# Performance work log

Measured on AMD Instinct MI355X. Metric: run time of the kernel, lower is better.

The kernel has to match this reference:

```python
import jax, jax.numpy as jnp
import numpy as np

N = 50000
E = 1600000
D_IN = 128
HID = 128
EPS = 1e-5
NEG_SLOPE = 0.2


def setup_inputs() -> dict:
    key = jax.random.key(0)
    ks = jax.random.split(key, 16)
    s = 1.0 / np.sqrt(D_IN)
    inp = {
        'x': jax.random.normal(ks[0], (N, D_IN), dtype=jnp.float32),
        'edge_index': jax.random.randint(ks[1], (2, E), 0, N, dtype=jnp.int64),
        # layer 0 params
        'W0': jax.random.normal(ks[2], (D_IN, HID), dtype=jnp.float32) * s,
        'att_src0': jax.random.normal(ks[3], (HID,), dtype=jnp.float32) * s,
        'att_dst0': jax.random.normal(ks[4], (HID,), dtype=jnp.float32) * s,
        'bias0': jnp.zeros((HID,), dtype=jnp.float32),
        'gamma0': jnp.ones((HID,), dtype=jnp.float32),
        'beta0': jnp.zeros((HID,), dtype=jnp.float32),
        # layer 1 params
        'W1': jax.random.normal(ks[5], (HID, HID), dtype=jnp.float32) * s,
        'att_src1': jax.random.normal(ks[6], (HID,), dtype=jnp.float32) * s,
        'att_dst1': jax.random.normal(ks[7], (HID,), dtype=jnp.float32) * s,
        'bias1': jnp.zeros((HID,), dtype=jnp.float32),
        'gamma1': jnp.ones((HID,), dtype=jnp.float32),
        'beta1': jnp.zeros((HID,), dtype=jnp.float32),
    }
    return inp


def _gat_conv(x, W, a_src, a_dst, bias, src, dst, n_nodes):
    h = x @ W                                   # [N, HID]
    alpha_src = h @ a_src                       # [N]
    alpha_dst = h @ a_dst                       # [N]
    e = jax.nn.leaky_relu(alpha_src[src] + alpha_dst[dst], NEG_SLOPE)  # [E']
    # numerically stable softmax over edges grouped by destination node
    m = jax.ops.segment_max(e, dst, num_segments=n_nodes)
    ex = jnp.exp(e - m[dst])
    denom = jax.ops.segment_sum(ex, dst, num_segments=n_nodes)
    alpha = ex / denom[dst]                     # [E']
    out = jax.ops.segment_sum(h[src] * alpha[:, None], dst, num_segments=n_nodes)
    return out + bias


def _batch_norm(x, gamma, beta):
    mean = jnp.mean(x, axis=0)
    var = jnp.mean(jnp.square(x - mean), axis=0)  # biased variance (torch BN normalization)
    return gamma * (x - mean) * jax.lax.rsqrt(var + EPS) + beta


def reference(x, edge_index, W0, att_src0, att_dst0, bias0, gamma0, beta0,
              W1, att_src1, att_dst1, bias1, gamma1, beta1):
    n = x.shape[0]
    loops = jnp.arange(n, dtype=edge_index.dtype)
    src = jnp.concatenate([edge_index[0], loops])
    dst = jnp.concatenate([edge_index[1], loops])

    h = _gat_conv(x, W0, att_src0, att_dst0, bias0, src, dst, n)
    h = _batch_norm(h, gamma0, beta0)
    h = jax.nn.relu(h)
    # dropout: identity in eval mode

    h = _gat_conv(h, W1, att_src1, att_dst1, bias1, src, dst, n)
    h = _batch_norm(h, gamma1, beta1)
    h = jax.nn.relu(h)  # last_activation=True
    return h
```

## Files before the change

kernel.cpp:

```cpp
#include <hip/hip_runtime.h>
#include <math.h>

#define HID 128
#define PAD 96
#define NB 196
#define CAP 10240
#define CHUNK 4096
#define AGG_BLOCKS 2048
#define NEG_SLOPE 0.2f
#define EPS 1e-5f

typedef __attribute__((ext_vector_type(8))) short short8;
typedef __attribute__((ext_vector_type(4))) float floatx4;

static __device__ __forceinline__ unsigned bf16_rne(float x) {
    unsigned u = __float_as_uint(x);
    return (u + 0x7fffu + ((u >> 16) & 1u)) >> 16;
}
static __device__ __forceinline__ float bf16lo_f(unsigned u) { return __uint_as_float(u << 16); }
static __device__ __forceinline__ float bf16hi_f(unsigned u) { return __uint_as_float(u & 0xffff0000u); }

__global__ void wt_build(const float* __restrict__ W, unsigned short* __restrict__ Wt,
                         unsigned short* __restrict__ Hb, int N) {
    int t = threadIdx.x;
    if (t < 64) ((unsigned*)(Hb + (size_t)N * HID))[t] = 0u;
    for (int task = t; task < 2048; task += 256) {
        int c = task & 127, k0 = (task >> 7) * 8;
        unsigned v[8];
#pragma unroll
        for (int j = 0; j < 8; ++j) v[j] = bf16_rne(W[(k0 + j) * HID + c]);
        uint4 st;
        st.x = v[0] | (v[1] << 16);
        st.y = v[2] | (v[3] << 16);
        st.z = v[4] | (v[5] << 16);
        st.w = v[6] | (v[7] << 16);
        *(uint4*)&Wt[c * HID + k0] = st;
    }
}

template <bool BN>
__global__ __launch_bounds__(256) void gemm_mfma(
    const float* __restrict__ X, const unsigned short* __restrict__ Wt,
    const float* __restrict__ a_src, const float* __restrict__ a_dst,
    const float* __restrict__ coef,
    unsigned short* __restrict__ Hb, float* __restrict__ asrc, float* __restrict__ adst,
    int N)
{
    int tid = threadIdx.x;
    int wv = tid >> 6, lane = tid & 63;
    int g = lane >> 4, c = lane & 15;
    int r0w = blockIdx.x * 64 + wv * 16;
    int arow = r0w + c;
    bool avalid = arow < N;
    const float* xr = X + (size_t)(avalid ? arow : 0) * HID;

    floatx4 acc[8];
#pragma unroll
    for (int i = 0; i < 8; ++i) acc[i] = (floatx4)0.f;

#pragma unroll
    for (int kc = 0; kc < 4; ++kc) {
        int k0 = kc * 32 + g * 8;
        float xv[8];
        float4 x0 = *(const float4*)&xr[k0];
        float4 x1 = *(const float4*)&xr[k0 + 4];
        xv[0] = x0.x; xv[1] = x0.y; xv[2] = x0.z; xv[3] = x0.w;
        xv[4] = x1.x; xv[5] = x1.y; xv[6] = x1.z; xv[7] = x1.w;
        if (BN) {
            float4 s0 = *(const float4*)&coef[k0];
            float4 s1 = *(const float4*)&coef[k0 + 4];
            float4 h0 = *(const float4*)&coef[HID + k0];
            float4 h1 = *(const float4*)&coef[HID + k0 + 4];
            xv[0] = fmaxf(fmaf(xv[0], s0.x, h0.x), 0.f);
            xv[1] = fmaxf(fmaf(xv[1], s0.y, h0.y), 0.f);
            xv[2] = fmaxf(fmaf(xv[2], s0.z, h0.z), 0.f);
            xv[3] = fmaxf(fmaf(xv[3], s0.w, h0.w), 0.f);
            xv[4] = fmaxf(fmaf(xv[4], s1.x, h1.x), 0.f);
            xv[5] = fmaxf(fmaf(xv[5], s1.y, h1.y), 0.f);
            xv[6] = fmaxf(fmaf(xv[6], s1.z, h1.z), 0.f);
            xv[7] = fmaxf(fmaf(xv[7], s1.w, h1.w), 0.f);
        }
        short8 af;
#pragma unroll
        for (int j = 0; j < 8; ++j) af[j] = avalid ? (short)bf16_rne(xv[j]) : (short)0;

#pragma unroll
        for (int nt = 0; nt < 8; ++nt) {
            short8 bf = *(const short8*)&Wt[(nt * 16 + c) * HID + k0];
            acc[nt] = __builtin_amdgcn_mfma_f32_16x16x32_bf16(af, bf, acc[nt], 0, 0, 0);
        }
    }

    float as_c[8], ad_c[8];
#pragma unroll
    for (int nt = 0; nt < 8; ++nt) {
        as_c[nt] = a_src[nt * 16 + c];
        ad_c[nt] = a_dst[nt * 16 + c];
    }
#pragma unroll
    for (int reg = 0; reg < 4; ++reg) {
        float s = 0.f, d = 0.f;
#pragma unroll
        for (int nt = 0; nt < 8; ++nt) {
            s = fmaf(acc[nt][reg], as_c[nt], s);
            d = fmaf(acc[nt][reg], ad_c[nt], d);
        }
#pragma unroll
        for (int o = 1; o < 16; o <<= 1) {
            s += __shfl_xor(s, o);
            d += __shfl_xor(d, o);
        }
        int crow = r0w + g * 4 + reg;
        if (c == 0 && crow < N) { asrc[crow] = s; adst[crow] = d; }
    }
#pragma unroll
    for (int reg = 0; reg < 4; ++reg) {
        int crow = r0w + g * 4 + reg;
        if (crow < N) {
#pragma unroll
            for (int nt = 0; nt < 8; ++nt)
                Hb[(size_t)crow * HID + nt * 16 + c] = (unsigned short)bf16_rne(acc[nt][reg]);
        }
    }
}

__global__ __launch_bounds__(256) void scatter_part(
    const int* __restrict__ ei, int* __restrict__ bcur,
    unsigned int* __restrict__ bbuf, int E)
{
    __shared__ int lcnt[NB], gbase[NB];
    int tid = threadIdx.x;
    int i0 = blockIdx.x * CHUNK;
    int i1 = i0 + CHUNK; if (i1 > E) i1 = E;
    if (tid < NB) lcnt[tid] = 0;
    __syncthreads();
    for (int i = i0 + tid; i < i1; i += 256)
        atomicAdd(&lcnt[ei[E + i] >> 8], 1);
    __syncthreads();
    if (tid < NB) {
        gbase[tid] = atomicAdd(&bcur[tid], lcnt[tid]);
        lcnt[tid] = 0;
    }
    __syncthreads();
    for (int i = i0 + tid; i < i1; i += 256) {
        int s = ei[i], d = ei[E + i];
        int b = d >> 8;
        int off = atomicAdd(&lcnt[b], 1);
        int pos = gbase[b] + off;
        if (pos < CAP)
            bbuf[(size_t)b * CAP + pos] = ((unsigned)s << 8) | (unsigned)(d & 255);
    }
}

__global__ __launch_bounds__(256) void ell_build(
    const unsigned int* __restrict__ bbuf, const int* __restrict__ bcur,
    int* __restrict__ cnt, int* __restrict__ ell, float* __restrict__ asrc, int N)
{
    __shared__ int stage[256 * PAD];
    __shared__ int scnt[256];
    int tid = threadIdx.x;
    int b = blockIdx.x;
    int base = b << 8;
    int nodes = N - base; if (nodes > 256) nodes = 256;

    if (b == 0 && tid == 0) asrc[N] = -1e30f;

    int4 s4; s4.x = s4.y = s4.z = s4.w = N;
    for (int idx = tid * 4; idx < 256 * PAD; idx += 1024)
        *(int4*)&stage[idx] = s4;
    __syncthreads();
    for (int i = tid; i < nodes; i += 256) {
        stage[i * PAD] = base + i;
        scnt[i] = 1;
    }
    __syncthreads();

    int nb = bcur[b]; if (nb > CAP) nb = CAP;
    const unsigned int* buf = bbuf + (size_t)b * CAP;
    for (int j = tid; j < nb; j += 256) {
        unsigned int v = buf[j];
        int dl = (int)(v & 255u);
        int s = (int)(v >> 8);
        int p = atomicAdd(&scnt[dl], 1);
        if (p < PAD) stage[dl * PAD + p] = s;
    }
    __syncthreads();

    int total = nodes * PAD;
    int* dst = ell + (size_t)base * PAD;
    for (int idx = tid * 4; idx < total; idx += 1024)
        *(int4*)&dst[idx] = *(const int4*)&stage[idx];
    for (int i = tid; i < nodes; i += 256)
        cnt[base + i] = scnt[i];
}

__global__ __launch_bounds__(256) void gat_aggregate(
    const unsigned short* __restrict__ Hb, const float* __restrict__ asrc,
    const float* __restrict__ adst, const int* __restrict__ cnt,
    const int* __restrict__ ell, const float* __restrict__ bias,
    float* __restrict__ OUT, float* __restrict__ stat, int N)
{
    __shared__ float sbuf[4][HID], qbuf[4][HID];
    int tid = threadIdx.x, wv = tid >> 6, lane = tid & 63;
    int h = lane >> 5, li = lane & 31;
    int c0 = 4 * li;
    float4 b4 = *(const float4*)&bias[c0];
    float ss0 = 0.f, ss1 = 0.f, ss2 = 0.f, ss3 = 0.f;
    float qq0 = 0.f, qq1 = 0.f, qq2 = 0.f, qq3 = 0.f;

    for (int n = blockIdx.x * 4 + wv; n < N; n += AGG_BLOCKS * 4) {
        int nn = __builtin_amdgcn_readfirstlane(n);
        int deg = cnt[nn]; if (deg > PAD) deg = PAD;
        const int* row = ell + (size_t)nn * PAD;
        float adn = adst[nn];
        float a0 = 0.f, a1 = 0.f, a2 = 0.f, a3 = 0.f, den = 0.f;

        for (int j = 0; j < deg; j += 16) {
            int4 s0 = *(const int4*)&row[j];
            int4 s1 = *(const int4*)&row[j + 4];
            int4 s2 = *(const int4*)&row[j + 8];
            int4 s3 = *(const int4*)&row[j + 12];
            int e0 = h ? s0.y : s0.x;
            int e1 = h ? s0.w : s0.z;
            int e2 = h ? s1.y : s1.x;
            int e3 = h ? s1.w : s1.z;
            int e4 = h ? s2.y : s2.x;
            int e5 = h ? s2.w : s2.z;
            int e6 = h ? s3.y : s3.x;
            int e7 = h ? s3.w : s3.z;
#define PAIR(SI) { int si = (SI);                                     \
            float v = asrc[si] + adn;                                 \
            v = fmaxf(v, v * NEG_SLOPE);                              \
            float w = __expf(v);                                      \
            den += w;                                                 \
            uint2 hv = *(const uint2*)(Hb + (size_t)si * HID + c0);   \
            a0 = fmaf(w, bf16lo_f(hv.x), a0);                         \
            a1 = fmaf(w, bf16hi_f(hv.x), a1);                         \
            a2 = fmaf(w, bf16lo_f(hv.y), a2);                         \
            a3 = fmaf(w, bf16hi_f(hv.y), a3); }
            PAIR(e0) PAIR(e1) PAIR(e2) PAIR(e3)
            PAIR(e4) PAIR(e5) PAIR(e6) PAIR(e7)
#undef PAIR
        }

        den += __shfl_xor(den, 32);
        a0 += __shfl_xor(a0, 32);
        a1 += __shfl_xor(a1, 32);
        a2 += __shfl_xor(a2, 32);
        a3 += __shfl_xor(a3, 32);

        float inv = 1.f / den;
        float o0 = fmaf(a0, inv, b4.x);
        float o1 = fmaf(a1, inv, b4.y);
        float o2 = fmaf(a2, inv, b4.z);
        float o3 = fmaf(a3, inv, b4.w);
        ss0 += o0; ss1 += o1; ss2 += o2; ss3 += o3;
        qq0 = fmaf(o0, o0, qq0); qq1 = fmaf(o1, o1, qq1);
        qq2 = fmaf(o2, o2, qq2); qq3 = fmaf(o3, o3, qq3);
        if (h == 0) {
            float4 st;
            st.x = o0; st.y = o1; st.z = o2; st.w = o3;
            *(float4*)&OUT[(size_t)nn * HID + c0] = st;
        }
    }

    if (h == 0) {
        sbuf[wv][c0] = ss0; sbuf[wv][c0 + 1] = ss1;
        sbuf[wv][c0 + 2] = ss2; sbuf[wv][c0 + 3] = ss3;
        qbuf[wv][c0] = qq0; qbuf[wv][c0 + 1] = qq1;
        qbuf[wv][c0 + 2] = qq2; qbuf[wv][c0 + 3] = qq3;
    }
    __syncthreads();
    if (tid < HID) {
        float t = sbuf[0][tid] + sbuf[1][tid] + sbuf[2][tid] + sbuf[3][tid];
        atomicAdd(&stat[tid], t);
    } else {
        int cc = tid - HID;
        float t = qbuf[0][cc] + qbuf[1][cc] + qbuf[2][cc] + qbuf[3][cc];
        atomicAdd(&stat[HID + cc], t);
    }
}

__global__ void bn_coef(const float* __restrict__ stat, const float* __restrict__ gamma,
                        const float* __restrict__ beta, float* __restrict__ coef,
                        float invN)
{
    int c = threadIdx.x;
    float mean = stat[c] * invN;
    float var = stat[HID + c] * invN - mean * mean;
    float s = gamma[c] * rsqrtf(var + EPS);
    coef[c] = s;
    coef[HID + c] = beta[c] - mean * s;
}

__global__ __launch_bounds__(256) void bn_apply(
    float* __restrict__ X, const float* __restrict__ coef, int N)
{
    int tid = threadIdx.x, lane = tid & 63, wv = tid >> 6;
    int c0 = 2 * lane;
    float s0 = coef[c0], s1 = coef[c0 + 1];
    float h0 = coef[HID + c0], h1 = coef[HID + c0 + 1];
    for (int r = blockIdx.x * 4 + wv; r < N; r += gridDim.x * 4) {
        float2 v = *(float2*)&X[(size_t)r * HID + c0];
        float y0 = fmaxf(fmaf(v.x, s0, h0), 0.f);
        float y1 = fmaxf(fmaf(v.y, s1, h1), 0.f);
        *(float2*)&X[(size_t)r * HID + c0] = make_float2(y0, y1);
    }
}

extern "C" void kernel_launch(void* const* d_in, const int* in_sizes, int n_in,
                              void* d_out, int out_size, void* d_ws, size_t ws_size,
                              hipStream_t stream)
{
    const float* x        = (const float*)d_in[0];
    const int*   ei       = (const int*)d_in[1];
    const float* W0       = (const float*)d_in[2];
    const float* att_src0 = (const float*)d_in[3];
    const float* att_dst0 = (const float*)d_in[4];
    const float* bias0    = (const float*)d_in[5];
    const float* gamma0   = (const float*)d_in[6];
    const float* beta0    = (const float*)d_in[7];
    const float* W1       = (const float*)d_in[8];
    const float* att_src1 = (const float*)d_in[9];
    const float* att_dst1 = (const float*)d_in[10];
    const float* bias1    = (const float*)d_in[11];
    const float* gamma1   = (const float*)d_in[12];
    const float* beta1    = (const float*)d_in[13];

    const int N = in_sizes[0] / HID;
    const int E = in_sizes[1] / 2;
    float* out = (float*)d_out;

    char* wsbase = (char*)d_ws;
    size_t off = 0;
    auto alloc = [&](size_t bytes) -> void* {
        void* p = wsbase + off;
        off += (bytes + 255) & ~(size_t)255;
        return p;
    };
    unsigned short* Hb   = (unsigned short*)alloc((size_t)(N + 1) * HID * 2);
    float*          asrc = (float*)alloc((size_t)(N + 1) * 4);
    float*          adst = (float*)alloc((size_t)N * 4);
    int*            cnt  = (int*)  alloc((size_t)N * 4);
    int*            ell  = (int*)  alloc((size_t)N * PAD * 4);
    unsigned int*   bbuf = (unsigned int*)alloc((size_t)NB * CAP * 4);
    int*            bcur = (int*)  alloc(NB * 4);
    float*          stats = (float*)alloc(4 * HID * 4);
    float*          coef0 = (float*)alloc(2 * HID * 4);
    float*          coef1 = (float*)alloc(2 * HID * 4);
    unsigned short* Wt0  = (unsigned short*)alloc(HID * HID * 2);
    unsigned short* Wt1  = (unsigned short*)alloc(HID * HID * 2);
    float* stat0 = stats;
    float* stat1 = stats + 2 * HID;

    const int gemm_blocks  = (N + 63) / 64;
    const int part_blocks  = (E + CHUNK - 1) / CHUNK;
    const int build_blocks = (N + 255) / 256;
    const float invN = 1.0f / (float)N;

    (void)hipMemsetAsync(bcur, 0, NB * 4, stream);
    (void)hipMemsetAsync(stats, 0, 4 * HID * 4, stream);

    wt_build<<<1, 256, 0, stream>>>(W0, Wt0, Hb, N);
    wt_build<<<1, 256, 0, stream>>>(W1, Wt1, Hb, N);
    scatter_part<<<part_blocks, 256, 0, stream>>>(ei, bcur, bbuf, E);
    ell_build<<<build_blocks, 256, 0, stream>>>(bbuf, bcur, cnt, ell, asrc, N);

    gemm_mfma<false><<<gemm_blocks, 256, 0, stream>>>(
        x, Wt0, att_src0, att_dst0, nullptr, Hb, asrc, adst, N);
    gat_aggregate<<<AGG_BLOCKS, 256, 0, stream>>>(
        Hb, asrc, adst, cnt, ell, bias0, out, stat0, N);
    bn_coef<<<1, HID, 0, stream>>>(stat0, gamma0, beta0, coef0, invN);

    gemm_mfma<true><<<gemm_blocks, 256, 0, stream>>>(
        out, Wt1, att_src1, att_dst1, coef0, Hb, asrc, adst, N);
    gat_aggregate<<<AGG_BLOCKS, 256, 0, stream>>>(
        Hb, asrc, adst, cnt, ell, bias1, out, stat1, N);
    bn_coef<<<1, HID, 0, stream>>>(stat1, gamma1, beta1, coef1, invN);
    bn_apply<<<2048, 256, 0, stream>>>(out, coef1, N);
}
```

Before: 289.9 us.

## Precompute packed per-edge attention weights before GAT aggregation

Adds an edge_w kernel that computes the leaky-ReLU exp attention weight for every padded ELL slot. It packs each weight as bf16 together with the 16-bit source index into one word. The aggregation kernel then reads these packed words, dropping its per-edge asrc gather and exp, and the aggregation grid size is doubled. In exchange the new kernel touches every padded slot, which is about three times the real edge count, and adds a full read and write of the ELL array per layer. It also narrows the weights to bf16 and relies on node indices fitting in 16 bits.

New measurement: 382.8 us. 32.1% more time.

```diff
diff --git a/kernel.cpp b/kernel.cpp
--- a/kernel.cpp
+++ b/kernel.cpp
@@ -6,7 +6,7 @@
 #define NB 196
 #define CAP 10240
 #define CHUNK 4096
-#define AGG_BLOCKS 2048
+#define AGG_BLOCKS 4096
 #define NEG_SLOPE 0.2f
 #define EPS 1e-5f
 
@@ -194,10 +194,23 @@
         cnt[base + i] = scnt[i];
 }
 
+__global__ __launch_bounds__(256) void edge_w(
+    const int* __restrict__ ell, const float* __restrict__ asrc,
+    const float* __restrict__ adst, unsigned* __restrict__ ellw, int total)
+{
+    int i = blockIdx.x * 256 + threadIdx.x;
+    if (i >= total) return;
+    int si = ell[i];
+    int node = i / PAD;
+    float v = asrc[si] + adst[node];
+    v = fmaxf(v, v * NEG_SLOPE);
+    float w = __expf(v);
+    ellw[i] = ((unsigned)si << 16) | bf16_rne(w);
+}
+
 __global__ __launch_bounds__(256) void gat_aggregate(
-    const unsigned short* __restrict__ Hb, const float* __restrict__ asrc,
-    const float* __restrict__ adst, const int* __restrict__ cnt,
-    const int* __restrict__ ell, const float* __restrict__ bias,
+    const unsigned short* __restrict__ Hb, const unsigned* __restrict__ ellw,
+    const int* __restrict__ cnt, const float* __restrict__ bias,
     float* __restrict__ OUT, float* __restrict__ stat, int N)
 {
     __shared__ float sbuf[4][HID], qbuf[4][HID];
@@ -211,27 +224,25 @@
     for (int n = blockIdx.x * 4 + wv; n < N; n += AGG_BLOCKS * 4) {
         int nn = __builtin_amdgcn_readfirstlane(n);
         int deg = cnt[nn]; if (deg > PAD) deg = PAD;
-        const int* row = ell + (size_t)nn * PAD;
-        float adn = adst[nn];
+        const unsigned* row = ellw + (size_t)nn * PAD;
         float a0 = 0.f, a1 = 0.f, a2 = 0.f, a3 = 0.f, den = 0.f;
 
         for (int j = 0; j < deg; j += 16) {
-            int4 s0 = *(const int4*)&row[j];
-            int4 s1 = *(const int4*)&row[j + 4];
-            int4 s2 = *(const int4*)&row[j + 8];
-            int4 s3 = *(const int4*)&row[j + 12];
-            int e0 = h ? s0.y : s0.x;
-            int e1 = h ? s0.w : s0.z;
-            int e2 = h ? s1.y : s1.x;
-            int e3 = h ? s1.w : s1.z;
-            int e4 = h ? s2.y : s2.x;
-            int e5 = h ? s2.w : s2.z;
-            int e6 = h ? s3.y : s3.x;
-            int e7 = h ? s3.w : s3.z;
-#define PAIR(SI) { int si = (SI);                                     \
-            float v = asrc[si] + adn;                                 \
-            v = fmaxf(v, v * NEG_SLOPE);                              \
-            float w = __expf(v);                                      \
+            uint4 s0 = *(const uint4*)&row[j];
+            uint4 s1 = *(const uint4*)&row[j + 4];
+            uint4 s2 = *(const uint4*)&row[j + 8];
+            uint4 s3 = *(const uint4*)&row[j + 12];
+            unsigned e0 = h ? s0.y : s0.x;
+            unsigned e1 = h ? s0.w : s0.z;
+            unsigned e2 = h ? s1.y : s1.x;
+            unsigned e3 = h ? s1.w : s1.z;
+            unsigned e4 = h ? s2.y : s2.x;
+            unsigned e5 = h ? s2.w : s2.z;
+            unsigned e6 = h ? s3.y : s3.x;
+            unsigned e7 = h ? s3.w : s3.z;
+#define PAIR(P) { unsigned p = (P);                                   \
+            float w = __uint_as_float(p << 16);                       \
+            int si = (int)(p >> 16);                                  \
             den += w;                                                 \
             uint2 hv = *(const uint2*)(Hb + (size_t)si * HID + c0);   \
             a0 = fmaf(w, bf16lo_f(hv.x), a0);                         \
@@ -343,6 +354,7 @@
     float*          adst = (float*)alloc((size_t)N * 4);
     int*            cnt  = (int*)  alloc((size_t)N * 4);
     int*            ell  = (int*)  alloc((size_t)N * PAD * 4);
+    unsigned*       ellw = (unsigned*)alloc((size_t)N * PAD * 4);
     unsigned int*   bbuf = (unsigned int*)alloc((size_t)NB * CAP * 4);
     int*            bcur = (int*)  alloc(NB * 4);
     float*          stats = (float*)alloc(4 * HID * 4);
@@ -356,6 +368,8 @@
     const int gemm_blocks  = (N + 63) / 64;
     const int part_blocks  = (E + CHUNK - 1) / CHUNK;
     const int build_blocks = (N + 255) / 256;
+    const int slots        = N * PAD;
+    const int ew_blocks    = (slots + 255) / 256;
     const float invN = 1.0f / (float)N;
 
     (void)hipMemsetAsync(bcur, 0, NB * 4, stream);
@@ -368,14 +382,16 @@
 
     gemm_mfma<false><<<gemm_blocks, 256, 0, stream>>>(
         x, Wt0, att_src0, att_dst0, nullptr, Hb, asrc, adst, N);
+    edge_w<<<ew_blocks, 256, 0, stream>>>(ell, asrc, adst, ellw, slots);
     gat_aggregate<<<AGG_BLOCKS, 256, 0, stream>>>(
-        Hb, asrc, adst, cnt, ell, bias0, out, stat0, N);
+        Hb, ellw, cnt, bias0, out, stat0, N);
     bn_coef<<<1, HID, 0, stream>>>(stat0, gamma0, beta0, coef0, invN);
 
     gemm_mfma<true><<<gemm_blocks, 256, 0, stream>>>(
         out, Wt1, att_src1, att_dst1, coef0, Hb, asrc, adst, N);
+    edge_w<<<ew_blocks, 256, 0, stream>>>(ell, asrc, adst, ellw, slots);
     gat_aggregate<<<AGG_BLOCKS, 256, 0, stream>>>(
-        Hb, asrc, adst, cnt, ell, bias1, out, stat1, N);
+        Hb, ellw, cnt, bias1, out, stat1, N);
     bn_coef<<<1, HID, 0, stream>>>(stat1, gamma1, beta1, coef1, invN);
     bn_apply<<<2048, 256, 0, stream>>>(out, coef1, N);
 }
```
